# Performance work log

Hardware: AMD Instinct MI355X
Metric: run time of the kernel (lower is better)

Reference implementation:

```python
import jax, jax.numpy as jnp
import numpy as np

HIDDEN = 1152
HEADS = 16
HEAD_DIM = HIDDEN // HEADS

def setup_inputs() -> dict:
    key = jax.random.key(0)
    ks = jax.random.split(key, 7)
    s = 1.0 / np.sqrt(HIDDEN)
    return {
        "x": jax.random.normal(ks[0], (16, 1024, HIDDEN), dtype=jnp.float32),
        "w_qkv": jax.random.normal(ks[1], (3 * HIDDEN, HIDDEN), dtype=jnp.float32) * s,
        "b_qkv": jax.random.normal(ks[2], (3 * HIDDEN,), dtype=jnp.float32) * 0.01,
        "q_gamma": jnp.ones((HEAD_DIM,), dtype=jnp.float32),
        "k_gamma": jnp.ones((HEAD_DIM,), dtype=jnp.float32),
        "w_proj": jax.random.normal(ks[3], (HIDDEN, HIDDEN), dtype=jnp.float32) * s,
        "b_proj": jax.random.normal(ks[4], (HIDDEN,), dtype=jnp.float32) * 0.01,
    }

def _rmsnorm(t, gamma):
    # normalize over last dim (head_dim); torch RMSNorm default eps = finfo(dtype).eps
    eps = jnp.asarray(jnp.finfo(t.dtype).eps, t.dtype)
    ms = jnp.mean(jnp.square(t), axis=-1, keepdims=True)
    return t * jax.lax.rsqrt(ms + eps) * gamma

def reference(x, w_qkv, b_qkv, q_gamma, k_gamma, w_proj, b_proj):
    B, S, H = x.shape
    qkv = x @ w_qkv.T + b_qkv                       # [B,S,3H]
    qkv = qkv.reshape(B, S, 3, HEADS, HEAD_DIM)
    qkv = jnp.transpose(qkv, (2, 0, 3, 1, 4))       # [3,B,nh,S,hd]
    q, k, v = qkv[0], qkv[1], qkv[2]
    q = _rmsnorm(q, q_gamma)
    k = _rmsnorm(k, k_gamma)
    scale = 1.0 / np.sqrt(HEAD_DIM)
    scores = jnp.einsum('bhqd,bhkd->bhqk', q, k) * scale
    probs = jax.nn.softmax(scores, axis=-1)
    out = jnp.einsum('bhqk,bhkd->bhqd', probs, v)   # [B,nh,S,hd]
    out = jnp.transpose(out, (0, 2, 1, 3)).reshape(B, S, H)
    return out @ w_proj.T + b_proj
```

## Files before the change

kernel.cpp:

```cpp
#include <hip/hip_runtime.h>

typedef _Float16 f16;
typedef _Float16 f16x8 __attribute__((ext_vector_type(8)));
typedef _Float16 f16x4 __attribute__((ext_vector_type(4)));
typedef float f32x4 __attribute__((ext_vector_type(4)));

__device__ __forceinline__ void gld16(const void* g, void* l) {
    __builtin_amdgcn_global_load_lds(
        (const __attribute__((address_space(1))) void*)g,
        (__attribute__((address_space(3))) void*)l,
        16, 0, 0);
}

__global__ __launch_bounds__(256) void f32_to_f16_vec(const float* __restrict__ in,
                                                      f16* __restrict__ out, long n4) {
    long i = (long)blockIdx.x * 256 + threadIdx.x;
    if (i < n4) {
        float4 v = ((const float4*)in)[i];
        f16x4 o = {(f16)v.x, (f16)v.y, (f16)v.z, (f16)v.w};
        ((f16x4*)out)[i] = o;
    }
}

constexpr int GEMM_BUF_E = 12288;

struct GPtrs {
    const f16 *a0, *a1, *a2, *a3, *b0, *b1;
};

__device__ __forceinline__ void stage6(f16* s, const GPtrs& g, int dA, int dB) {
    gld16(g.a0, s + dA);
    gld16(g.a1, s + dA + 2048);
    gld16(g.a2, s + dA + 4096);
    gld16(g.a3, s + dA + 6144);
    gld16(g.b0, s + dB);
    gld16(g.b1, s + dB + 2048);
}

template<int BUF, bool STG>
__device__ __forceinline__ void tile_step(f16* sm, GPtrs& g,
                                          int dA, int dB,
                                          int offA, int offB,
                                          f32x4 (&acc)[8][4]) {
    const f16* bp = sm + BUF * GEMM_BUF_E;
    if (STG) {
        constexpr int SB = (BUF + 2) % 3;
        stage6(sm + SB * GEMM_BUF_E, g, dA, dB);
        g.a0 += 32; g.a1 += 32; g.a2 += 32; g.a3 += 32;
        g.b0 += 32; g.b1 += 32;
    }
    f16x8 bf[4], af[4], ag[4];
#pragma unroll
    for (int nt = 0; nt < 4; ++nt) bf[nt] = *(const f16x8*)(bp + offB + nt * 512);
#pragma unroll
    for (int mt = 0; mt < 4; ++mt) af[mt] = *(const f16x8*)(bp + offA + mt * 512);
#pragma unroll
    for (int mt = 0; mt < 4; ++mt) ag[mt] = *(const f16x8*)(bp + offA + 2048 + mt * 512);
    __builtin_amdgcn_s_setprio(1);
#pragma unroll
    for (int mt = 0; mt < 4; ++mt)
#pragma unroll
        for (int nt = 0; nt < 4; ++nt)
            acc[mt][nt] = __builtin_amdgcn_mfma_f32_16x16x32_f16(
                af[mt], bf[nt], acc[mt][nt], 0, 0, 0);
#pragma unroll
    for (int mt = 0; mt < 4; ++mt)
#pragma unroll
        for (int nt = 0; nt < 4; ++nt)
            acc[4 + mt][nt] = __builtin_amdgcn_mfma_f32_16x16x32_f16(
                ag[mt], bf[nt], acc[4 + mt][nt], 0, 0, 0);
    __builtin_amdgcn_s_setprio(0);
}

__global__ __launch_bounds__(256, 2) void gemm8(const f16* __restrict__ A,
                                                const f16* __restrict__ B,
                                                const float* __restrict__ bias,
                                                float* __restrict__ Cf,
                                                f16* __restrict__ Ch,
                                                int M, int N, int K) {
    __shared__ f16 sm[3 * GEMM_BUF_E];
    const int tid = threadIdx.x;
    const int w = tid >> 6, lane = tid & 63;
    const int quad = lane >> 4, l16 = lane & 15;
    const int wm = w >> 1, wn = w & 1;

    const int nnb = N >> 7;
    const int mpx = (M >> 8) >> 3;
    const int xcd = blockIdx.x & 7;
    const int s = blockIdx.x >> 3;
    const int mband = s / nnb;
    const int nblk = s - mband * nnb;
    const long m0 = (long)(xcd * mpx + mband) << 8;
    const long n0 = (long)nblk << 7;

    const int r4 = lane >> 2;
    const int sc = ((lane & 3) ^ ((lane >> 3) & 3)) << 3;
    GPtrs g;
    g.a0 = A + (m0 +   0 + w * 16 + r4) * (long)K + sc;
    g.a1 = A + (m0 +  64 + w * 16 + r4) * (long)K + sc;
    g.a2 = A + (m0 + 128 + w * 16 + r4) * (long)K + sc;
    g.a3 = A + (m0 + 192 + w * 16 + r4) * (long)K + sc;
    g.b0 = B + (n0 +   0 + w * 16 + r4) * (long)K + sc;
    g.b1 = B + (n0 +  64 + w * 16 + r4) * (long)K + sc;
    const int dA = __builtin_amdgcn_readfirstlane(w * 512);
    const int dB = __builtin_amdgcn_readfirstlane(8192 + w * 512);

    const int swz = (quad ^ ((l16 >> 1) & 3)) << 3;
    const int offA = (wm * 128 + l16) * 32 + swz;
    const int offB = 8192 + (wn * 64 + l16) * 32 + swz;

    f32x4 acc[8][4] = {};

    stage6(sm, g, dA, dB);
    {
        GPtrs g1 = g;
        g1.a0 += 32; g1.a1 += 32; g1.a2 += 32; g1.a3 += 32; g1.b0 += 32; g1.b1 += 32;
        stage6(sm + GEMM_BUF_E, g1, dA, dB);
    }
    g.a0 += 64; g.a1 += 64; g.a2 += 64; g.a3 += 64; g.b0 += 64; g.b1 += 64;
    asm volatile("s_waitcnt vmcnt(6)" ::: "memory");
    __builtin_amdgcn_s_barrier();
    __builtin_amdgcn_sched_barrier(0);

#define VMB(NSTR) asm volatile("s_waitcnt vmcnt(" NSTR ")" ::: "memory"); \
                  __builtin_amdgcn_s_barrier();                           \
                  __builtin_amdgcn_sched_barrier(0);

#pragma unroll 1
    for (int it = 0; it < 11; ++it) {
        tile_step<0, true>(sm, g, dA, dB, offA, offB, acc); VMB("6")
        tile_step<1, true>(sm, g, dA, dB, offA, offB, acc); VMB("6")
        tile_step<2, true>(sm, g, dA, dB, offA, offB, acc); VMB("6")
    }
    tile_step<0, true >(sm, g, dA, dB, offA, offB, acc); VMB("6")
    tile_step<1, false>(sm, g, dA, dB, offA, offB, acc); VMB("0")
    tile_step<2, false>(sm, g, dA, dB, offA, offB, acc);
#undef VMB

    float bv[4];
#pragma unroll
    for (int nt = 0; nt < 4; ++nt)
        bv[nt] = bias ? bias[n0 + wn * 64 + nt * 16 + l16] : 0.f;
#pragma unroll
    for (int mt = 0; mt < 8; ++mt) {
#pragma unroll
        for (int r = 0; r < 4; ++r) {
            const long row = m0 + wm * 128 + mt * 16 + quad * 4 + r;
#pragma unroll
            for (int nt = 0; nt < 4; ++nt) {
                const long col = n0 + wn * 64 + nt * 16 + l16;
                const float v = acc[mt][nt][r] + bv[nt];
                if (Ch) Ch[row * (long)N + col] = (f16)v;
                else    Cf[row * (long)N + col] = v;
            }
        }
    }
}

__global__ __launch_bounds__(256) void qk_norm2(f16* __restrict__ qkv,
                                                const float* __restrict__ qg,
                                                const float* __restrict__ kg,
                                                f16* __restrict__ kc) {
    const float QSCALE = 0.117851130198f;
    const int t = blockIdx.x * 256 + threadIdx.x;
    const int h = t & 15;
    const long bs = t >> 4;
    f16* qp = qkv + bs * 3456 + h * 72;
    {
        f16x8 v[9];
        float ss = 0.f;
#pragma unroll
        for (int c = 0; c < 9; ++c) {
            v[c] = *(const f16x8*)(qp + c * 8);
#pragma unroll
            for (int j = 0; j < 8; ++j) { float f = (float)v[c][j]; ss += f * f; }
        }
        const float rs = rsqrtf(ss * (1.f / 72.f) + 1.1920928955078125e-7f) * QSCALE;
#pragma unroll
        for (int c = 0; c < 9; ++c) {
            f16x8 o;
#pragma unroll
            for (int j = 0; j < 8; ++j) o[j] = (f16)((float)v[c][j] * rs * qg[c * 8 + j]);
            *(f16x8*)(qp + c * 8) = o;
        }
    }
    {
        const f16* kp = qp + 1152;
        f16* dst = kc + ((long)((bs >> 10) * 16 + h) * 1024 + (bs & 1023)) * 72;
        f16x8 v[9];
        float ss = 0.f;
#pragma unroll
        for (int c = 0; c < 9; ++c) {
            v[c] = *(const f16x8*)(kp + c * 8);
#pragma unroll
            for (int j = 0; j < 8; ++j) { float f = (float)v[c][j]; ss += f * f; }
        }
        const float rs = rsqrtf(ss * (1.f / 72.f) + 1.1920928955078125e-7f);
#pragma unroll
        for (int c = 0; c < 9; ++c) {
            f16x8 o;
#pragma unroll
            for (int j = 0; j < 8; ++j) o[j] = (f16)((float)v[c][j] * rs * kg[c * 8 + j]);
            *(f16x8*)(dst + c * 8) = o;
        }
    }
}

__global__ __launch_bounds__(256) void vt_kernel(const f16* __restrict__ QKV,
                                                 f16* __restrict__ Vt) {
    __shared__ f16 tile[64][73];
    const int tid = threadIdx.x;
    const int bh = blockIdx.x;
    const int b = bh >> 4, h = bh & 15;
    const int s0 = blockIdx.y * 64;
    for (int idx = tid; idx < 64 * 72; idx += 256) {
        const int r = idx / 72, c = idx % 72;
        tile[r][c] = QKV[((long)(b * 1024 + s0 + r)) * 3456 + 2304 + h * 72 + c];
    }
    __syncthreads();
    for (int idx = tid; idx < 72 * 64; idx += 256) {
        const int d = idx >> 6, s = idx & 63;
        Vt[((long)bh * 72 + d) * 1024 + s0 + s] = tile[s][d];
    }
}

__global__ __launch_bounds__(256) void attn2(const f16* __restrict__ QKV,
                                             const f16* __restrict__ Kc,
                                             const f16* __restrict__ Vt,
                                             f16* __restrict__ O) {
    constexpr int S = 1024;
    constexpr int KSZ = 64 * 72;
    constexpr int VSZ = 80 * 76;
    __shared__ f16 smem[2 * KSZ + 2 * VSZ];
    f16* KsA = smem;
    f16* VsA = smem + 2 * KSZ;
    const int tid = threadIdx.x;
    const int w = tid >> 6, lane = tid & 63;
    const int quad = lane >> 4, l16 = lane & 15;

    const int b = blockIdx.x;
    const int xcd = b & 7;
    const int j = b >> 3;
    const int bh = ((j >> 3) << 3) | xcd;
    const int qt = j & 7;
    const int bb = bh >> 4, h = bh & 15;
    const int q0 = qt * 128;

    for (int i = tid; i < 8 * 76; i += 256) {
        const int pr = i / 76, pc = i % 76;
        const f16 pv = (pr == 0 && pc < 64) ? (f16)1.f : (f16)0.f;
        VsA[(72 + pr) * 76 + pc] = pv;
        VsA[VSZ + (72 + pr) * 76 + pc] = pv;
    }

    const f16* qrow0 = QKV + ((long)(bb * 1024 + q0 + w * 32 + l16)) * 3456 + h * 72;
    const f16* qrow1 = qrow0 + (long)16 * 3456;
    f16x8 qz = {};
    f16x8 qf[2][3];
    qf[0][0] = *(const f16x8*)(qrow0 + quad * 8);
    qf[0][1] = *(const f16x8*)(qrow0 + 32 + quad * 8);
    qf[0][2] = (quad == 0) ? *(const f16x8*)(qrow0 + 64) : qz;
    qf[1][0] = *(const f16x8*)(qrow1 + quad * 8);
    qf[1][1] = *(const f16x8*)(qrow1 + 32 + quad * 8);
    qf[1][2] = (quad == 0) ? *(const f16x8*)(qrow1 + 64) : qz;

    f32x4 o[2][5] = {};

    const f16* gK = Kc + (long)bh * S * 72;
    const f16* gV = Vt + (long)bh * 72 * S;

    f16x8 vr[3];

    for (int ch = w; ch < 9; ch += 4)
        gld16(gK + ch * 512 + lane * 8,
              &KsA[__builtin_amdgcn_readfirstlane(ch * 512)]);
#pragma unroll
    for (int it = 0; it < 3; ++it) {
        const int idx = it * 256 + tid;
        if (idx < 576)
            vr[it] = *(const f16x8*)(gV + (long)(idx >> 3) * 1024 + (idx & 7) * 8);
    }
#pragma unroll
    for (int it = 0; it < 3; ++it) {
        const int idx = it * 256 + tid;
        if (idx < 576) {
            const int d = idx >> 3, s8 = (idx & 7) * 8;
            f16x4 lo = {vr[it][0], vr[it][1], vr[it][2], vr[it][3]};
            f16x4 hi = {vr[it][4], vr[it][5], vr[it][6], vr[it][7]};
            *(f16x4*)&VsA[d * 76 + s8] = lo;
            *(f16x4*)&VsA[d * 76 + s8 + 4] = hi;
        }
    }
    __syncthreads();

#pragma unroll 1
    for (int t = 0; t < 16; ++t) {
        const int buf = t & 1;
        const f16* Ks = KsA + buf * KSZ;
        const f16* Vs = VsA + buf * VSZ;

        if (t < 15) {
            const int s1 = (t + 1) * 64;
            for (int ch = w; ch < 9; ch += 4)
                gld16(gK + (long)s1 * 72 + ch * 512 + lane * 8,
                      &KsA[__builtin_amdgcn_readfirstlane((buf ^ 1) * KSZ + ch * 512)]);
#pragma unroll
            for (int it = 0; it < 3; ++it) {
                const int idx = it * 256 + tid;
                if (idx < 576)
                    vr[it] = *(const f16x8*)(gV + (long)(idx >> 3) * 1024 + s1 + (idx & 7) * 8);
            }
        }

        f32x4 sc[4][2] = {};
        __builtin_amdgcn_s_setprio(1);
#pragma unroll
        for (int ss = 0; ss < 4; ++ss) {
            const int base = (ss * 16 + l16) * 72;
            f16x8 k0 = *(const f16x8*)&Ks[base + quad * 8];
            f16x8 k1 = *(const f16x8*)&Ks[base + 32 + quad * 8];
            f16x8 k2 = *(const f16x8*)&Ks[base + 64 + quad * 8];
            sc[ss][0] = __builtin_amdgcn_mfma_f32_16x16x32_f16(k0, qf[0][0], sc[ss][0], 0, 0, 0);
            sc[ss][0] = __builtin_amdgcn_mfma_f32_16x16x32_f16(k1, qf[0][1], sc[ss][0], 0, 0, 0);
            sc[ss][0] = __builtin_amdgcn_mfma_f32_16x16x32_f16(k2, qf[0][2], sc[ss][0], 0, 0, 0);
            sc[ss][1] = __builtin_amdgcn_mfma_f32_16x16x32_f16(k0, qf[1][0], sc[ss][1], 0, 0, 0);
            sc[ss][1] = __builtin_amdgcn_mfma_f32_16x16x32_f16(k1, qf[1][1], sc[ss][1], 0, 0, 0);
            sc[ss][1] = __builtin_amdgcn_mfma_f32_16x16x32_f16(k2, qf[1][2], sc[ss][1], 0, 0, 0);
        }
        __builtin_amdgcn_s_setprio(0);

        f16x4 pf[4][2];
#pragma unroll
        for (int ss = 0; ss < 4; ++ss)
#pragma unroll
            for (int qs = 0; qs < 2; ++qs) {
                f16x4 pk;
#pragma unroll
                for (int r = 0; r < 4; ++r) pk[r] = (f16)__expf(sc[ss][qs][r]);
                pf[ss][qs] = pk;
            }

        __builtin_amdgcn_s_setprio(1);
#pragma unroll
        for (int vt = 0; vt < 5; ++vt) {
#pragma unroll
            for (int ss = 0; ss < 4; ++ss) {
                f16x4 vf = *(const f16x4*)&Vs[(vt * 16 + l16) * 76 + ss * 16 + quad * 4];
                o[0][vt] = __builtin_amdgcn_mfma_f32_16x16x16f16(vf, pf[ss][0], o[0][vt], 0, 0, 0);
                o[1][vt] = __builtin_amdgcn_mfma_f32_16x16x16f16(vf, pf[ss][1], o[1][vt], 0, 0, 0);
            }
        }
        __builtin_amdgcn_s_setprio(0);

        if (t < 15) {
#pragma unroll
            for (int it = 0; it < 3; ++it) {
                const int idx = it * 256 + tid;
                if (idx < 576) {
                    const int d = idx >> 3, s8 = (idx & 7) * 8;
                    f16x4 lo = {vr[it][0], vr[it][1], vr[it][2], vr[it][3]};
                    f16x4 hi = {vr[it][4], vr[it][5], vr[it][6], vr[it][7]};
                    *(f16x4*)&VsA[(buf ^ 1) * VSZ + d * 76 + s8] = lo;
                    *(f16x4*)&VsA[(buf ^ 1) * VSZ + d * 76 + s8 + 4] = hi;
                }
            }
        }
        __syncthreads();
    }

    const float l0 = __shfl(o[0][4][0], 32 + l16);
    const float l1 = __shfl(o[1][4][0], 32 + l16);
    const float inv[2] = {1.f / l0, 1.f / l1};

    f16* es = smem + w * 2560;
#pragma unroll
    for (int qs = 0; qs < 2; ++qs) {
        f16* row = es + (qs * 16 + l16) * 80;
#pragma unroll
        for (int vt = 0; vt < 5; ++vt)
#pragma unroll
            for (int r = 0; r < 4; ++r) {
                const int d = vt * 16 + quad * 4 + r;
                if (d < 72) row[d] = (f16)(o[qs][vt][r] * inv[qs]);
            }
    }
    const long rowbase = (long)bb * 1024 + q0 + w * 32;
#pragma unroll
    for (int it = 0; it < 5; ++it) {
        const int idx = it * 64 + lane;
        if (idx < 288) {
            const int q = idx / 9, c = idx - q * 9;
            f16x4 a = *(const f16x4*)&es[q * 80 + c * 8];
            f16x4 b2 = *(const f16x4*)&es[q * 80 + c * 8 + 4];
            f16* dst = O + (rowbase + q) * 1152 + h * 72 + c * 8;
            *(f16x4*)dst = a;
            *(f16x4*)(dst + 4) = b2;
        }
    }
}

extern "C" void kernel_launch(void* const* d_in, const int* in_sizes, int n_in,
                              void* d_out, int out_size, void* d_ws, size_t ws_size,
                              hipStream_t stream) {
    const float* x       = (const float*)d_in[0];
    const float* w_qkv   = (const float*)d_in[1];
    const float* b_qkv   = (const float*)d_in[2];
    const float* q_gamma = (const float*)d_in[3];
    const float* k_gamma = (const float*)d_in[4];
    const float* w_proj  = (const float*)d_in[5];
    const float* b_proj  = (const float*)d_in[6];
    float* out = (float*)d_out;

    char* p = (char*)d_ws;
    f16* x_h = (f16*)p;      p += (size_t)16384 * 1152 * 2;
    f16* wqkv_h = (f16*)p;   p += (size_t)3456 * 1152 * 2;
    f16* wproj_h = (f16*)p;  p += (size_t)1152 * 1152 * 2;
    f16* qkv_h = (f16*)p;    p += (size_t)16384 * 3456 * 2;
    const size_t needed = (size_t)(p - (char*)d_ws);
    if (ws_size < needed) return;

    f16* k_c = (f16*)d_out;
    f16* v_t = (f16*)d_out + (size_t)16384 * 1152;

    f32_to_f16_vec<<<18432, 256, 0, stream>>>(x, x_h, 16384L * 1152 / 4);
    f32_to_f16_vec<<<3888, 256, 0, stream>>>(w_qkv, wqkv_h, 3456L * 1152 / 4);
    f32_to_f16_vec<<<1296, 256, 0, stream>>>(w_proj, wproj_h, 1152L * 1152 / 4);

    gemm8<<<1728, 256, 0, stream>>>(
        x_h, wqkv_h, b_qkv, nullptr, qkv_h, 16384, 3456, 1152);

    qk_norm2<<<1024, 256, 0, stream>>>(qkv_h, q_gamma, k_gamma, k_c);
    vt_kernel<<<dim3(256, 16), 256, 0, stream>>>(qkv_h, v_t);

    attn2<<<2048, 256, 0, stream>>>(qkv_h, k_c, v_t, x_h );

    gemm8<<<576, 256, 0, stream>>>(
        x_h, wproj_h, b_proj, out, nullptr, 16384, 1152, 1152);
}
```

Measured before the change: 516.2 us.

## Software-pipeline LDS fragment loads in GEMM and vectorize V transpose

The GEMM main loop now loads the next tile's LDS fragments right after the barrier and issues the MFMAs for the current tile on registers already loaded. This overlaps LDS reads with the MFMA chain and the global-to-LDS staging, at the cost of more live fragment registers. Separately, the V-transpose kernel switches to 16-byte vector loads and stores with a padded 80-wide LDS tile. The padding may raise LDS bank conflicts on the column reads.

```diff
diff --git a/kernel.cpp b/kernel.cpp
--- a/kernel.cpp
+++ b/kernel.cpp
@@ -28,47 +28,36 @@
     const f16 *a0, *a1, *a2, *a3, *b0, *b1;
 };
 
-__device__ __forceinline__ void stage6(f16* s, const GPtrs& g, int dA, int dB) {
+__device__ __forceinline__ void stage6(f16* s, GPtrs& g, int dA, int dB) {
     gld16(g.a0, s + dA);
     gld16(g.a1, s + dA + 2048);
     gld16(g.a2, s + dA + 4096);
     gld16(g.a3, s + dA + 6144);
     gld16(g.b0, s + dB);
     gld16(g.b1, s + dB + 2048);
-}
-
-template<int BUF, bool STG>
-__device__ __forceinline__ void tile_step(f16* sm, GPtrs& g,
-                                          int dA, int dB,
-                                          int offA, int offB,
-                                          f32x4 (&acc)[8][4]) {
+    g.a0 += 32; g.a1 += 32; g.a2 += 32; g.a3 += 32;
+    g.b0 += 32; g.b1 += 32;
+}
+
+template<int BUF>
+__device__ __forceinline__ void ld_frags(const f16* sm, int offA, int offB,
+                                         f16x8 (&fa)[8], f16x8 (&fb)[4]) {
     const f16* bp = sm + BUF * GEMM_BUF_E;
-    if (STG) {
-        constexpr int SB = (BUF + 2) % 3;
-        stage6(sm + SB * GEMM_BUF_E, g, dA, dB);
-        g.a0 += 32; g.a1 += 32; g.a2 += 32; g.a3 += 32;
-        g.b0 += 32; g.b1 += 32;
-    }
-    f16x8 bf[4], af[4], ag[4];
-#pragma unroll
-    for (int nt = 0; nt < 4; ++nt) bf[nt] = *(const f16x8*)(bp + offB + nt * 512);
-#pragma unroll
-    for (int mt = 0; mt < 4; ++mt) af[mt] = *(const f16x8*)(bp + offA + mt * 512);
-#pragma unroll
-    for (int mt = 0; mt < 4; ++mt) ag[mt] = *(const f16x8*)(bp + offA + 2048 + mt * 512);
+#pragma unroll
+    for (int nt = 0; nt < 4; ++nt) fb[nt] = *(const f16x8*)(bp + offB + nt * 512);
+#pragma unroll
+    for (int mt = 0; mt < 8; ++mt) fa[mt] = *(const f16x8*)(bp + offA + mt * 512);
+}
+
+__device__ __forceinline__ void mfma16(const f16x8 (&fa)[8], const f16x8 (&fb)[4],
+                                       f32x4 (&acc)[8][4]) {
     __builtin_amdgcn_s_setprio(1);
 #pragma unroll
-    for (int mt = 0; mt < 4; ++mt)
+    for (int mt = 0; mt < 8; ++mt)
 #pragma unroll
         for (int nt = 0; nt < 4; ++nt)
             acc[mt][nt] = __builtin_amdgcn_mfma_f32_16x16x32_f16(
-                af[mt], bf[nt], acc[mt][nt], 0, 0, 0);
-#pragma unroll
-    for (int mt = 0; mt < 4; ++mt)
-#pragma unroll
-        for (int nt = 0; nt < 4; ++nt)
-            acc[4 + mt][nt] = __builtin_amdgcn_mfma_f32_16x16x32_f16(
-                ag[mt], bf[nt], acc[4 + mt][nt], 0, 0, 0);
+                fa[mt], fb[nt], acc[mt][nt], 0, 0, 0);
     __builtin_amdgcn_s_setprio(0);
 }
 
@@ -110,32 +99,31 @@
     const int offB = 8192 + (wn * 64 + l16) * 32 + swz;
 
     f32x4 acc[8][4] = {};
+    f16x8 fa[8];
+    f16x8 fb[4];
 
     stage6(sm, g, dA, dB);
-    {
-        GPtrs g1 = g;
-        g1.a0 += 32; g1.a1 += 32; g1.a2 += 32; g1.a3 += 32; g1.b0 += 32; g1.b1 += 32;
-        stage6(sm + GEMM_BUF_E, g1, dA, dB);
-    }
-    g.a0 += 64; g.a1 += 64; g.a2 += 64; g.a3 += 64; g.b0 += 64; g.b1 += 64;
+    stage6(sm + GEMM_BUF_E, g, dA, dB);
     asm volatile("s_waitcnt vmcnt(6)" ::: "memory");
     __builtin_amdgcn_s_barrier();
     __builtin_amdgcn_sched_barrier(0);
-
-#define VMB(NSTR) asm volatile("s_waitcnt vmcnt(" NSTR ")" ::: "memory"); \
-                  __builtin_amdgcn_s_barrier();                           \
-                  __builtin_amdgcn_sched_barrier(0);
+    ld_frags<0>(sm, offA, offB, fa, fb);
+
+#define BND(VN, NB) asm volatile("s_waitcnt vmcnt(" VN ")" ::: "memory"); \
+                    __builtin_amdgcn_s_barrier();                         \
+                    __builtin_amdgcn_sched_barrier(0);                    \
+                    ld_frags<NB>(sm, offA, offB, fa, fb);
 
 #pragma unroll 1
     for (int it = 0; it < 11; ++it) {
-        tile_step<0, true>(sm, g, dA, dB, offA, offB, acc); VMB("6")
-        tile_step<1, true>(sm, g, dA, dB, offA, offB, acc); VMB("6")
-        tile_step<2, true>(sm, g, dA, dB, offA, offB, acc); VMB("6")
-    }
-    tile_step<0, true >(sm, g, dA, dB, offA, offB, acc); VMB("6")
-    tile_step<1, false>(sm, g, dA, dB, offA, offB, acc); VMB("0")
-    tile_step<2, false>(sm, g, dA, dB, offA, offB, acc);
-#undef VMB
+        stage6(sm + 2 * GEMM_BUF_E, g, dA, dB); mfma16(fa, fb, acc); BND("6", 1)
+        stage6(sm + 0 * GEMM_BUF_E, g, dA, dB); mfma16(fa, fb, acc); BND("6", 2)
+        stage6(sm + 1 * GEMM_BUF_E, g, dA, dB); mfma16(fa, fb, acc); BND("6", 0)
+    }
+    stage6(sm + 2 * GEMM_BUF_E, g, dA, dB); mfma16(fa, fb, acc); BND("6", 1)
+    mfma16(fa, fb, acc); BND("0", 2)
+    mfma16(fa, fb, acc);
+#undef BND
 
     float bv[4];
 #pragma unroll
@@ -208,19 +196,23 @@
 
 __global__ __launch_bounds__(256) void vt_kernel(const f16* __restrict__ QKV,
                                                  f16* __restrict__ Vt) {
-    __shared__ f16 tile[64][73];
+    __shared__ f16 tile[64][80];
     const int tid = threadIdx.x;
     const int bh = blockIdx.x;
     const int b = bh >> 4, h = bh & 15;
     const int s0 = blockIdx.y * 64;
-    for (int idx = tid; idx < 64 * 72; idx += 256) {
-        const int r = idx / 72, c = idx % 72;
-        tile[r][c] = QKV[((long)(b * 1024 + s0 + r)) * 3456 + 2304 + h * 72 + c];
+    for (int idx = tid; idx < 576; idx += 256) {
+        const int r = idx / 9, c = idx % 9;
+        *(f16x8*)&tile[r][c * 8] =
+            *(const f16x8*)&QKV[((long)(b * 1024 + s0 + r)) * 3456 + 2304 + h * 72 + c * 8];
     }
     __syncthreads();
-    for (int idx = tid; idx < 72 * 64; idx += 256) {
-        const int d = idx >> 6, s = idx & 63;
-        Vt[((long)bh * 72 + d) * 1024 + s0 + s] = tile[s][d];
+    for (int idx = tid; idx < 576; idx += 256) {
+        const int d = idx >> 3, sg = (idx & 7) * 8;
+        f16x8 o;
+#pragma unroll
+        for (int j = 0; j < 8; ++j) o[j] = tile[sg + j][d];
+        *(f16x8*)&Vt[((long)bh * 72 + d) * 1024 + s0 + sg] = o;
     }
 }
 
```

New measurement: 1.865 ms. +261.4%, slower.
